# Performance work log

Measured on AMD Instinct MI355X. Metric: run time of the kernel, lower is better.

## Reference

```python
import jax, jax.numpy as jnp
import numpy as np

T, B, I, H, L = 512, 64, 1024, 1024, 2


def setup_inputs() -> dict:
    key = jax.random.key(0)
    ks = jax.random.split(key, 10)
    stdv = 1.0 / np.sqrt(H)
    u = lambda k, shape: jax.random.uniform(k, shape, jnp.float32, -stdv, stdv)
    return {
        "x": jax.random.normal(ks[0], (T, B, I), jnp.float32),
        "hx": jnp.zeros((L, B, H), jnp.float32),
        "cx": jnp.zeros((L, B, H), jnp.float32),
        "w_ih0": u(ks[1], (4 * H, I)),
        "w_hh0": u(ks[2], (4 * H, H)),
        "b_ih0": u(ks[3], (4 * H,)),
        "b_hh0": u(ks[4], (4 * H,)),
        "w_ih1": u(ks[5], (4 * H, H)),
        "w_hh1": u(ks[6], (4 * H, H)),
        "b_ih1": u(ks[7], (4 * H,)),
        "b_hh1": u(ks[8], (4 * H,)),
    }


def _lstm_layer(x, h0, c0, w_ih, w_hh, b_ih, b_hh):
    # Precompute input contribution for all timesteps: [T, B, 4H]
    igates = jnp.einsum("tbi,gi->tbg", x, w_ih) + b_ih

    def step(carry, ig_t):
        h, c = carry
        gates = ig_t + h @ w_hh.T + b_hh
        i, f, g, o = jnp.split(gates, 4, axis=-1)
        i = jax.nn.sigmoid(i)
        f = jax.nn.sigmoid(f)
        g = jnp.tanh(g)
        o = jax.nn.sigmoid(o)
        c = f * c + i * g
        h = o * jnp.tanh(c)
        return (h, c), h

    (hT, cT), out = jax.lax.scan(step, (h0, c0), igates)
    return out, hT, cT


def reference(x, hx, cx, w_ih0, w_hh0, b_ih0, b_hh0, w_ih1, w_hh1, b_ih1, b_hh1):
    params = [(w_ih0, w_hh0, b_ih0, b_hh0), (w_ih1, w_hh1, b_ih1, b_hh1)]
    out = x
    h_final, c_final = [], []
    for layer in range(L):
        out, hT, cT = _lstm_layer(out, hx[layer], cx[layer], *params[layer])
        h_final.append(hT)
        c_final.append(cT)
    hn = jnp.stack(h_final)  # [L, B, H]
    cn = jnp.stack(c_final)  # [L, B, H]
    return out, (hn, cn)
```

## Files before the change

kernel.cpp:

```cpp
#include <hip/hip_runtime.h>
#include <hip/hip_bf16.h>
#include <hip/hip_cooperative_groups.h>
#include <cstddef>

namespace cg = cooperative_groups;

typedef short bf16x8 __attribute__((ext_vector_type(8)));
typedef float f32x4 __attribute__((ext_vector_type(4)));

#define T_STEPS 512
#define BATCH   64
#define DIM     1024
#define BD      (BATCH*DIM)
#define XB_ELEMS ((size_t)T_STEPS*BATCH*DIM)
#define IGSLOT  262144
#define FSTRIDE 16

__device__ __forceinline__ float sigmoidf_(float x) { return 1.f / (1.f + __expf(-x)); }
__device__ __forceinline__ float tanhf_(float x)    { return 2.f / (1.f + __expf(-2.f * x)) - 1.f; }
__device__ __forceinline__ unsigned short f2bf(float f) {
    union { float f; unsigned int u; } v; v.f = f;
    unsigned int u = v.u + 0x7fffu + ((v.u >> 16) & 1u);
    return (unsigned short)(u >> 16);
}

__device__ __forceinline__ unsigned long long coh_load8(const void* p) {
    return __hip_atomic_load((const unsigned long long*)p,
                             __ATOMIC_RELAXED, __HIP_MEMORY_SCOPE_AGENT);
}
__device__ __forceinline__ void coh_store8(void* p, unsigned long long v) {
    __hip_atomic_store((unsigned long long*)p, v,
                       __ATOMIC_RELAXED, __HIP_MEMORY_SCOPE_AGENT);
}

__global__ void __launch_bounds__(512, 2)
lstm_fused(const float* __restrict__ x,
           const float* __restrict__ hx,
           const float* __restrict__ cx,
           const float* __restrict__ w_ih0, const float* __restrict__ w_hh0,
           const float* __restrict__ b_ih0, const float* __restrict__ b_hh0,
           const float* __restrict__ w_ih1, const float* __restrict__ w_hh1,
           const float* __restrict__ b_ih1, const float* __restrict__ b_hh1,
           float* __restrict__ out,
           unsigned short* __restrict__ ws)
{
    unsigned short* xb = ws;
    unsigned short* h0 = ws + XB_ELEMS;
    unsigned short* h1 = h0 + 4 * BD;
    float* ig0 = (float*)(h1 + 2 * BD);
    float* ig1 = ig0 + 2 * IGSLOT;
    unsigned* flags = (unsigned*)(ig1 + 2 * IGSLOT);

    const int tid  = threadIdx.x;
    const int lane = tid & 63;
    const int wave = tid >> 6;
    const int kw   = wave >> 2;
    const int mw   = wave & 3;
    const int bid  = blockIdx.x;
    const int role = bid >> 6;
    const int ug   = bid & 63;
    const int ub   = ug * 16;

    __shared__ __align__(16) unsigned short wB[65536];
    __shared__ __align__(16) unsigned short hstage[64][16];
    __shared__ __align__(16) f32x4 red[4][4][64];

    {
        const float* wm = (role == 0) ? w_ih0 : (role == 1) ? w_hh0
                        : (role == 2) ? w_ih1 : w_hh1;
        for (int idx = tid; idx < 8192; idx += 512) {
            int l  = idx & 63;
            int kc = (idx >> 6) & 31;
            int n  = idx >> 11;
            int c  = l & 15, kq = l >> 4;
            const float* src = wm + (size_t)(n * DIM + ub + c) * DIM + kc * 32 + kq * 8;
            float4 v0 = *(const float4*)(src);
            float4 v1 = *(const float4*)(src + 4);
            unsigned short o[8];
            o[0]=f2bf(v0.x); o[1]=f2bf(v0.y); o[2]=f2bf(v0.z); o[3]=f2bf(v0.w);
            o[4]=f2bf(v1.x); o[5]=f2bf(v1.y); o[6]=f2bf(v1.z); o[7]=f2bf(v1.w);
            *(bf16x8*)(&wB[(size_t)idx * 8]) = *(const bf16x8*)o;
        }
    }

    {
        const int nthr = 512 * gridDim.x;
        const int gtid = bid * 512 + tid;
        const float4* xv = (const float4*)x;
        const int n4 = (int)(XB_ELEMS / 4);
        for (int i = gtid; i < n4; i += nthr) {
            float4 v = xv[i];
            ushort4 o;
            o.x=f2bf(v.x); o.y=f2bf(v.y); o.z=f2bf(v.z); o.w=f2bf(v.w);
            *(ushort4*)(xb + (size_t)i * 4) = o;
        }
    }

    if (role == 1 || role == 3) {
        unsigned short* hdst = (role == 1) ? (h0 + 3 * BD) : (h1 + 1 * BD);
        const float* hsrc = hx + (size_t)(role >> 1) * BD;
        const int kcp0 = ub >> 5, sub0 = ub & 31;
        for (int e = tid; e < 1024; e += 512) {
            int row = e >> 4, uu = e & 15;
            hdst[kcp0 * 2048 + row * 32 + sub0 + uu] = f2bf(hsrc[row * DIM + ub + uu]);
        }
    }

    if (tid == 0)
        __hip_atomic_store(flags + (size_t)((role << 6) | ug) * FSTRIDE, 0u,
                           __ATOMIC_RELAXED, __HIP_MEMORY_SCOPE_AGENT);

    const int col  = lane & 15;
    const int quad = lane >> 4;

    float biasv[4] = {0.f, 0.f, 0.f, 0.f};
    if ((role == 0 || role == 2) && kw == 0) {
        const float* bi = (role == 0) ? b_ih0 : b_ih1;
        const float* bh = (role == 0) ? b_hh0 : b_hh1;
        #pragma unroll
        for (int n = 0; n < 4; ++n) {
            int row = n * DIM + ub + col;
            biasv[n] = bi[row] + bh[row];
        }
    }

    float creg[4] = {0.f, 0.f, 0.f, 0.f};
    if ((role == 1 || role == 3) && kw == 0) {
        const float* csrc = cx + (size_t)(role >> 1) * BD;
        #pragma unroll
        for (int r = 0; r < 4; ++r) {
            int m = mw * 16 + quad * 4 + r;
            creg[r] = csrc[m * DIM + ub + col];
        }
    }

    cg::grid_group grid = cg::this_grid();
    __syncthreads();
    grid.sync();

    const int arow = mw * 16 + col;
    const int kc0  = kw * 16;

    auto poll_ge = [&](const unsigned* f, int target) {
        while ((int)__hip_atomic_load(f, __ATOMIC_RELAXED, __HIP_MEMORY_SCOPE_AGENT) < target)
            __builtin_amdgcn_s_sleep(1);
    };
    auto Fp = [&](int set, int idx) -> unsigned* {
        return flags + (size_t)((set << 6) | idx) * FSTRIDE;
    };
    auto publish = [&](int set, int idx, int val) {
        __hip_atomic_store(Fp(set, idx), (unsigned)val,
                           __ATOMIC_RELAXED, __HIP_MEMORY_SCOPE_AGENT);
    };

    auto gemm_plain = [&](const unsigned short* Ap,
                          f32x4& A0, f32x4& A1, f32x4& A2, f32x4& A3) {
        const unsigned short* Abase = Ap + (size_t)arow * DIM + quad * 8 + kc0 * 32;
        #pragma unroll 8
        for (int k2 = 0; k2 < 16; ++k2) {
            int kc = kc0 + k2;
            bf16x8 a  = *(const bf16x8*)(Abase + k2 * 32);
            bf16x8 b0 = *(const bf16x8*)(&wB[((size_t)(0*32 + kc)*64 + lane)*8]);
            bf16x8 b1 = *(const bf16x8*)(&wB[((size_t)(1*32 + kc)*64 + lane)*8]);
            bf16x8 b2 = *(const bf16x8*)(&wB[((size_t)(2*32 + kc)*64 + lane)*8]);
            bf16x8 b3 = *(const bf16x8*)(&wB[((size_t)(3*32 + kc)*64 + lane)*8]);
            A0 = __builtin_amdgcn_mfma_f32_16x16x32_bf16(a, b0, A0, 0, 0, 0);
            A1 = __builtin_amdgcn_mfma_f32_16x16x32_bf16(a, b1, A1, 0, 0, 0);
            A2 = __builtin_amdgcn_mfma_f32_16x16x32_bf16(a, b2, A2, 0, 0, 0);
            A3 = __builtin_amdgcn_mfma_f32_16x16x32_bf16(a, b3, A3, 0, 0, 0);
        }
    };

    auto gemm_coh = [&](const unsigned short* Ap, const float* igb,
                        f32x4& A0, f32x4& A1, f32x4& A2, f32x4& A3) {
        const unsigned short* Abase = Ap + (size_t)arow * 32 + quad * 8
                                    + (size_t)kc0 * 2048;
        if (igb) {
            union { f32x4 v; unsigned long long q[2]; } g0, g1, g2, g3;
            g0.q[0] = coh_load8(igb + 0*128); g0.q[1] = coh_load8(igb + 1*128);
            g1.q[0] = coh_load8(igb + 2*128); g1.q[1] = coh_load8(igb + 3*128);
            g2.q[0] = coh_load8(igb + 4*128); g2.q[1] = coh_load8(igb + 5*128);
            g3.q[0] = coh_load8(igb + 6*128); g3.q[1] = coh_load8(igb + 7*128);
            A0 = g0.v; A1 = g1.v; A2 = g2.v; A3 = g3.v;
        }
        union U { bf16x8 v; unsigned long long q[2]; };
        U pre[8];
        #pragma unroll
        for (int i = 0; i < 8; ++i) {
            pre[i].q[0] = coh_load8(Abase + (size_t)i * 2048);
            pre[i].q[1] = coh_load8(Abase + (size_t)i * 2048 + 4);
        }
        #pragma unroll
        for (int k2 = 0; k2 < 16; ++k2) {
            U cur = pre[k2 & 7];
            if (k2 < 8) {
                pre[k2 & 7].q[0] = coh_load8(Abase + (size_t)(k2 + 8) * 2048);
                pre[k2 & 7].q[1] = coh_load8(Abase + (size_t)(k2 + 8) * 2048 + 4);
            }
            int kc = kc0 + k2;
            bf16x8 b0 = *(const bf16x8*)(&wB[((size_t)(0*32 + kc)*64 + lane)*8]);
            bf16x8 b1 = *(const bf16x8*)(&wB[((size_t)(1*32 + kc)*64 + lane)*8]);
            bf16x8 b2 = *(const bf16x8*)(&wB[((size_t)(2*32 + kc)*64 + lane)*8]);
            bf16x8 b3 = *(const bf16x8*)(&wB[((size_t)(3*32 + kc)*64 + lane)*8]);
            A0 = __builtin_amdgcn_mfma_f32_16x16x32_bf16(cur.v, b0, A0, 0, 0, 0);
            A1 = __builtin_amdgcn_mfma_f32_16x16x32_bf16(cur.v, b1, A1, 0, 0, 0);
            A2 = __builtin_amdgcn_mfma_f32_16x16x32_bf16(cur.v, b2, A2, 0, 0, 0);
            A3 = __builtin_amdgcn_mfma_f32_16x16x32_bf16(cur.v, b3, A3, 0, 0, 0);
        }
    };

    auto k_reduce = [&](f32x4& A0, f32x4& A1, f32x4& A2, f32x4& A3) {
        if (kw) {
            red[0][mw][lane] = A0; red[1][mw][lane] = A1;
            red[2][mw][lane] = A2; red[3][mw][lane] = A3;
        }
        __syncthreads();
        if (!kw) {
            A0 += red[0][mw][lane]; A1 += red[1][mw][lane];
            A2 += red[2][mw][lane]; A3 += red[3][mw][lane];
        }
    };

    auto dump_ig = [&](float* slot, int set, int t,
                       f32x4 A0, f32x4 A1, f32x4 A2, f32x4 A3) {
        if (!kw) {
            float* base = slot + (size_t)ug * 4096 + (size_t)mw * 1024 + lane * 2;
            union { f32x4 v; unsigned long long q[2]; } u0, u1, u2, u3;
            u0.v = A0; u1.v = A1; u2.v = A2; u3.v = A3;
            coh_store8(base + 0*128, u0.q[0]); coh_store8(base + 1*128, u0.q[1]);
            coh_store8(base + 2*128, u1.q[0]); coh_store8(base + 3*128, u1.q[1]);
            coh_store8(base + 4*128, u2.q[0]); coh_store8(base + 5*128, u2.q[1]);
            coh_store8(base + 6*128, u3.q[0]); coh_store8(base + 7*128, u3.q[1]);
        }
        asm volatile("s_waitcnt vmcnt(0)" ::: "memory");
        __syncthreads();
        if (tid == 0) publish(set, ug, t + 1);
    };

    const int kcp = ub >> 5, sub = ub & 31;

    for (int t = 0; t < T_STEPS; ++t) {
        f32x4 A0 = {0,0,0,0}, A1 = {0,0,0,0}, A2 = {0,0,0,0}, A3 = {0,0,0,0};

        if (role == 0) {
            if (tid == 0) poll_ge(Fp(1, ug), t - 1);
            __syncthreads();
            if (!kw) {
                A0 = f32x4{biasv[0], biasv[0], biasv[0], biasv[0]};
                A1 = f32x4{biasv[1], biasv[1], biasv[1], biasv[1]};
                A2 = f32x4{biasv[2], biasv[2], biasv[2], biasv[2]};
                A3 = f32x4{biasv[3], biasv[3], biasv[3], biasv[3]};
            }
            gemm_plain(xb + (size_t)t * BD, A0, A1, A2, A3);
            k_reduce(A0, A1, A2, A3);
            dump_ig(ig0 + (size_t)(t & 1) * IGSLOT, 0, t, A0, A1, A2, A3);

        } else if (role == 2) {
            if (tid < 64) poll_ge(Fp(1, tid), t + 1);
            else if (tid == 64) poll_ge(Fp(3, ug), t - 1);
            __syncthreads();
            if (!kw) {
                A0 = f32x4{biasv[0], biasv[0], biasv[0], biasv[0]};
                A1 = f32x4{biasv[1], biasv[1], biasv[1], biasv[1]};
                A2 = f32x4{biasv[2], biasv[2], biasv[2], biasv[2]};
                A3 = f32x4{biasv[3], biasv[3], biasv[3], biasv[3]};
            }
            gemm_coh(h0 + (size_t)(t & 3) * BD, nullptr, A0, A1, A2, A3);
            k_reduce(A0, A1, A2, A3);
            dump_ig(ig1 + (size_t)(t & 1) * IGSLOT, 2, t, A0, A1, A2, A3);

        } else {
            if (role == 1) {
                if (tid < 64) poll_ge(Fp(1, tid), t);
                else if (tid < 128) poll_ge(Fp(2, tid - 64), t - 3);
                else if (tid == 128) poll_ge(Fp(0, ug), t + 1);
            } else {
                if (tid < 64) poll_ge(Fp(3, tid), t);
                else if (tid == 64) poll_ge(Fp(2, ug), t + 1);
            }
            __syncthreads();

            unsigned short* hring = (role == 1) ? h0 : h1;
            const unsigned short* hsrc = (role == 1)
                ? (h0 + (size_t)((t - 1) & 3) * BD)
                : (h1 + (size_t)((t - 1) & 1) * BD);
            const float* igb = (!kw)
                ? ((role == 1) ? ig0 : ig1) + (size_t)(t & 1) * IGSLOT
                  + (size_t)ug * 4096 + (size_t)mw * 1024 + lane * 2
                : nullptr;
            gemm_coh(hsrc, igb, A0, A1, A2, A3);
            k_reduce(A0, A1, A2, A3);

            float hreg[4] = {0.f, 0.f, 0.f, 0.f};
            if (!kw) {
                #pragma unroll
                for (int r = 0; r < 4; ++r) {
                    float ig_ = sigmoidf_(A0[r]);
                    float fg_ = sigmoidf_(A1[r]);
                    float gg_ = tanhf_(A2[r]);
                    float og_ = sigmoidf_(A3[r]);
                    float c   = fg_ * creg[r] + ig_ * gg_;
                    creg[r]   = c;
                    float h   = og_ * tanhf_(c);
                    hreg[r]   = h;
                    int m = mw * 16 + quad * 4 + r;
                    hstage[m][col] = f2bf(h);
                }
            }
            __syncthreads();
            unsigned short* hout = hring
                + (size_t)((role == 1) ? (t & 3) : (t & 1)) * BD;
            if (wave == 0) {
                const unsigned long long* src = (const unsigned long long*)&hstage[lane][0];
                unsigned long long v0 = src[0], v1 = src[1], v2 = src[2], v3 = src[3];
                unsigned short* dst = hout + (size_t)kcp * 2048 + (size_t)lane * 32 + sub;
                coh_store8(dst + 0,  v0);
                coh_store8(dst + 4,  v1);
                coh_store8(dst + 8,  v2);
                coh_store8(dst + 12, v3);
                asm volatile("s_waitcnt vmcnt(0)" ::: "memory");
                if (tid == 0) publish(role, ug, t + 1);
            }

            if (!kw) {
                if (role == 3) {
                    #pragma unroll
                    for (int r = 0; r < 4; ++r) {
                        int m = mw * 16 + quad * 4 + r;
                        out[(size_t)t * BD + (size_t)m * DIM + ub + col] = hreg[r];
                        if (t == T_STEPS - 1) {
                            out[(size_t)T_STEPS * BD + 1 * BD + m * DIM + ub + col] = hreg[r];
                            out[(size_t)T_STEPS * BD + 3 * BD + m * DIM + ub + col] = creg[r];
                        }
                    }
                } else if (t == T_STEPS - 1) {
                    #pragma unroll
                    for (int r = 0; r < 4; ++r) {
                        int m = mw * 16 + quad * 4 + r;
                        out[(size_t)T_STEPS * BD + 0 * BD + m * DIM + ub + col] = hreg[r];
                        out[(size_t)T_STEPS * BD + 2 * BD + m * DIM + ub + col] = creg[r];
                    }
                }
            }
        }
    }
}

extern "C" void kernel_launch(void* const* d_in, const int* in_sizes, int n_in,
                              void* d_out, int out_size, void* d_ws, size_t ws_size,
                              hipStream_t stream) {
    const float* x     = (const float*)d_in[0];
    const float* hx    = (const float*)d_in[1];
    const float* cx    = (const float*)d_in[2];
    const float* w_ih0 = (const float*)d_in[3];
    const float* w_hh0 = (const float*)d_in[4];
    const float* b_ih0 = (const float*)d_in[5];
    const float* b_hh0 = (const float*)d_in[6];
    const float* w_ih1 = (const float*)d_in[7];
    const float* w_hh1 = (const float*)d_in[8];
    const float* b_ih1 = (const float*)d_in[9];
    const float* b_hh1 = (const float*)d_in[10];
    float* outp = (float*)d_out;
    unsigned short* wsp = (unsigned short*)d_ws;

    void* args[] = { &x, &hx, &cx, &w_ih0, &w_hh0, &b_ih0, &b_hh0,
                     &w_ih1, &w_hh1, &b_ih1, &b_hh1, &outp, &wsp };
    hipLaunchCooperativeKernel((void*)lstm_fused, dim3(256), dim3(512),
                               args, 0, stream);
}
```

Baseline: 3.548 ms.

## Replace block barriers with per-wave counter flags and shuffle-based h publishing

Cross-block synchronisation changes from one thread storing a step index to every wave atomically incrementing a counter, so consumers wait for a count of 4 per step. Polling now happens inside the waves that need the data, and most block-wide __syncthreads around polling and publishing are removed. The k-split reduction uses a workgroup-scope LDS counter instead of a second barrier. The h output is packed with wave shuffles instead of an LDS staging buffer. This aims to cut barrier latency on the serial recurrence path, but it adds more global atomics and relies on subtle memory ordering through relaxed atomics.

Result: slower. 4.593 ms (+29.5%).

```diff
diff --git a/kernel.cpp b/kernel.cpp
--- a/kernel.cpp
+++ b/kernel.cpp
@@ -62,8 +62,10 @@
     const int ub   = ug * 16;
 
     __shared__ __align__(16) unsigned short wB[65536];
-    __shared__ __align__(16) unsigned short hstage[64][16];
     __shared__ __align__(16) f32x4 red[4][4][64];
+    __shared__ unsigned cnt_rd;
+
+    if (tid == 0) cnt_rd = 0;
 
     {
         const float* wm = (role == 0) ? w_ih0 : (role == 1) ? w_hh0
@@ -141,16 +143,14 @@
     const int arow = mw * 16 + col;
     const int kc0  = kw * 16;
 
-    auto poll_ge = [&](const unsigned* f, int target) {
+    auto poll_cnt = [&](int set, int idx, int target) {
+        const unsigned* f = flags + (size_t)((set << 6) | idx) * FSTRIDE;
         while ((int)__hip_atomic_load(f, __ATOMIC_RELAXED, __HIP_MEMORY_SCOPE_AGENT) < target)
             __builtin_amdgcn_s_sleep(1);
     };
-    auto Fp = [&](int set, int idx) -> unsigned* {
-        return flags + (size_t)((set << 6) | idx) * FSTRIDE;
-    };
-    auto publish = [&](int set, int idx, int val) {
-        __hip_atomic_store(Fp(set, idx), (unsigned)val,
-                           __ATOMIC_RELAXED, __HIP_MEMORY_SCOPE_AGENT);
+    auto cnt_add = [&](int set, int idx) {
+        __hip_atomic_fetch_add(flags + (size_t)((set << 6) | idx) * FSTRIDE, 1u,
+                               __ATOMIC_RELAXED, __HIP_MEMORY_SCOPE_AGENT);
     };
 
     auto gemm_plain = [&](const unsigned short* Ap,
@@ -209,8 +209,11 @@
         }
     };
 
-    auto k_reduce = [&](f32x4& A0, f32x4& A1, f32x4& A2, f32x4& A3) {
+    auto k_reduce = [&](int t, f32x4& A0, f32x4& A1, f32x4& A2, f32x4& A3) {
         if (kw) {
+            while ((int)__hip_atomic_load(&cnt_rd, __ATOMIC_RELAXED,
+                                          __HIP_MEMORY_SCOPE_WORKGROUP) < 4 * t)
+                __builtin_amdgcn_s_sleep(1);
             red[0][mw][lane] = A0; red[1][mw][lane] = A1;
             red[2][mw][lane] = A2; red[3][mw][lane] = A3;
         }
@@ -218,23 +221,24 @@
         if (!kw) {
             A0 += red[0][mw][lane]; A1 += red[1][mw][lane];
             A2 += red[2][mw][lane]; A3 += red[3][mw][lane];
-        }
-    };
-
-    auto dump_ig = [&](float* slot, int set, int t,
+            asm volatile("s_waitcnt lgkmcnt(0)" ::: "memory");
+            if (lane == 0)
+                __hip_atomic_fetch_add(&cnt_rd, 1u, __ATOMIC_RELAXED,
+                                       __HIP_MEMORY_SCOPE_WORKGROUP);
+        }
+    };
+
+    auto dump_ig = [&](float* slot, int set,
                        f32x4 A0, f32x4 A1, f32x4 A2, f32x4 A3) {
-        if (!kw) {
-            float* base = slot + (size_t)ug * 4096 + (size_t)mw * 1024 + lane * 2;
-            union { f32x4 v; unsigned long long q[2]; } u0, u1, u2, u3;
-            u0.v = A0; u1.v = A1; u2.v = A2; u3.v = A3;
-            coh_store8(base + 0*128, u0.q[0]); coh_store8(base + 1*128, u0.q[1]);
-            coh_store8(base + 2*128, u1.q[0]); coh_store8(base + 3*128, u1.q[1]);
-            coh_store8(base + 4*128, u2.q[0]); coh_store8(base + 5*128, u2.q[1]);
-            coh_store8(base + 6*128, u3.q[0]); coh_store8(base + 7*128, u3.q[1]);
-        }
+        float* base = slot + (size_t)ug * 4096 + (size_t)mw * 1024 + lane * 2;
+        union { f32x4 v; unsigned long long q[2]; } u0, u1, u2, u3;
+        u0.v = A0; u1.v = A1; u2.v = A2; u3.v = A3;
+        coh_store8(base + 0*128, u0.q[0]); coh_store8(base + 1*128, u0.q[1]);
+        coh_store8(base + 2*128, u1.q[0]); coh_store8(base + 3*128, u1.q[1]);
+        coh_store8(base + 4*128, u2.q[0]); coh_store8(base + 5*128, u2.q[1]);
+        coh_store8(base + 6*128, u3.q[0]); coh_store8(base + 7*128, u3.q[1]);
         asm volatile("s_waitcnt vmcnt(0)" ::: "memory");
-        __syncthreads();
-        if (tid == 0) publish(set, ug, t + 1);
+        if (lane == 0) cnt_add(set, ug);
     };
 
     const int kcp = ub >> 5, sub = ub & 31;
@@ -243,8 +247,7 @@
         f32x4 A0 = {0,0,0,0}, A1 = {0,0,0,0}, A2 = {0,0,0,0}, A3 = {0,0,0,0};
 
         if (role == 0) {
-            if (tid == 0) poll_ge(Fp(1, ug), t - 1);
-            __syncthreads();
+            if (!kw && lane == 0) poll_cnt(1, ug, 4 * (t - 1));
             if (!kw) {
                 A0 = f32x4{biasv[0], biasv[0], biasv[0], biasv[0]};
                 A1 = f32x4{biasv[1], biasv[1], biasv[1], biasv[1]};
@@ -252,33 +255,42 @@
                 A3 = f32x4{biasv[3], biasv[3], biasv[3], biasv[3]};
             }
             gemm_plain(xb + (size_t)t * BD, A0, A1, A2, A3);
-            k_reduce(A0, A1, A2, A3);
-            dump_ig(ig0 + (size_t)(t & 1) * IGSLOT, 0, t, A0, A1, A2, A3);
+            k_reduce(t, A0, A1, A2, A3);
+            if (!kw) dump_ig(ig0 + (size_t)(t & 1) * IGSLOT, 0, A0, A1, A2, A3);
 
         } else if (role == 2) {
-            if (tid < 64) poll_ge(Fp(1, tid), t + 1);
-            else if (tid == 64) poll_ge(Fp(3, ug), t - 1);
-            __syncthreads();
             if (!kw) {
+                if (lane < 32) poll_cnt(1, lane, 4 * (t + 1));
+                else if (lane == 32) poll_cnt(3, ug, 4 * (t - 1));
                 A0 = f32x4{biasv[0], biasv[0], biasv[0], biasv[0]};
                 A1 = f32x4{biasv[1], biasv[1], biasv[1], biasv[1]};
                 A2 = f32x4{biasv[2], biasv[2], biasv[2], biasv[2]};
                 A3 = f32x4{biasv[3], biasv[3], biasv[3], biasv[3]};
+            } else {
+                if (lane < 32) poll_cnt(1, 32 + lane, 4 * (t + 1));
             }
             gemm_coh(h0 + (size_t)(t & 3) * BD, nullptr, A0, A1, A2, A3);
-            k_reduce(A0, A1, A2, A3);
-            dump_ig(ig1 + (size_t)(t & 1) * IGSLOT, 2, t, A0, A1, A2, A3);
+            k_reduce(t, A0, A1, A2, A3);
+            if (!kw) dump_ig(ig1 + (size_t)(t & 1) * IGSLOT, 2, A0, A1, A2, A3);
 
         } else {
             if (role == 1) {
-                if (tid < 64) poll_ge(Fp(1, tid), t);
-                else if (tid < 128) poll_ge(Fp(2, tid - 64), t - 3);
-                else if (tid == 128) poll_ge(Fp(0, ug), t + 1);
+                if (!kw) {
+                    if (lane < 32) poll_cnt(1, lane, 4 * t);
+                    else { poll_cnt(2, 2*(lane-32),     4*(t-3));
+                           poll_cnt(2, 2*(lane-32) + 1, 4*(t-3)); }
+                    if (lane == 0) poll_cnt(0, ug, 4 * (t + 1));
+                } else {
+                    if (lane < 32) poll_cnt(1, 32 + lane, 4 * t);
+                }
             } else {
-                if (tid < 64) poll_ge(Fp(3, tid), t);
-                else if (tid == 64) poll_ge(Fp(2, ug), t + 1);
-            }
-            __syncthreads();
+                if (!kw) {
+                    if (lane < 32) poll_cnt(3, lane, 4 * t);
+                    else if (lane == 32) poll_cnt(2, ug, 4 * (t + 1));
+                } else {
+                    if (lane < 32) poll_cnt(3, 32 + lane, 4 * t);
+                }
+            }
 
             unsigned short* hring = (role == 1) ? h0 : h1;
             const unsigned short* hsrc = (role == 1)
@@ -289,10 +301,10 @@
                   + (size_t)ug * 4096 + (size_t)mw * 1024 + lane * 2
                 : nullptr;
             gemm_coh(hsrc, igb, A0, A1, A2, A3);
-            k_reduce(A0, A1, A2, A3);
-
-            float hreg[4] = {0.f, 0.f, 0.f, 0.f};
+            k_reduce(t, A0, A1, A2, A3);
+
             if (!kw) {
+                float hreg[4];
                 #pragma unroll
                 for (int r = 0; r < 4; ++r) {
                     float ig_ = sigmoidf_(A0[r]);
@@ -301,44 +313,48 @@
                     float og_ = sigmoidf_(A3[r]);
                     float c   = fg_ * creg[r] + ig_ * gg_;
                     creg[r]   = c;
-                    float h   = og_ * tanhf_(c);
-                    hreg[r]   = h;
-                    int m = mw * 16 + quad * 4 + r;
-                    hstage[m][col] = f2bf(h);
-                }
-            }
-            __syncthreads();
-            unsigned short* hout = hring
-                + (size_t)((role == 1) ? (t & 3) : (t & 1)) * BD;
-            if (wave == 0) {
-                const unsigned long long* src = (const unsigned long long*)&hstage[lane][0];
-                unsigned long long v0 = src[0], v1 = src[1], v2 = src[2], v3 = src[3];
-                unsigned short* dst = hout + (size_t)kcp * 2048 + (size_t)lane * 32 + sub;
-                coh_store8(dst + 0,  v0);
-                coh_store8(dst + 4,  v1);
-                coh_store8(dst + 8,  v2);
-                coh_store8(dst + 12, v3);
+                    hreg[r]   = og_ * tanhf_(c);
+                }
+
+                unsigned short* hout = hring
+                    + (size_t)((role == 1) ? (t & 3) : (t & 1)) * BD;
+                int rw = lane >> 2, c4 = lane & 3;
+                int q2 = rw >> 2, r2 = rw & 3;
+                union { unsigned short u[4]; unsigned long long q; } pk;
+                #pragma unroll
+                for (int j = 0; j < 4; ++j) {
+                    int s = q2 * 16 + 4 * c4 + j;
+                    float v0s = __shfl(hreg[0], s);
+                    float v1s = __shfl(hreg[1], s);
+                    float v2s = __shfl(hreg[2], s);
+                    float v3s = __shfl(hreg[3], s);
+                    float v = (r2 == 0) ? v0s : (r2 == 1) ? v1s
+                            : (r2 == 2) ? v2s : v3s;
+                    pk.u[j] = f2bf(v);
+                }
+                int m = mw * 16 + rw;
+                unsigned short* dst = hout + (size_t)kcp * 2048
+                                    + (size_t)m * 32 + sub + 4 * c4;
+                coh_store8(dst, pk.q);
                 asm volatile("s_waitcnt vmcnt(0)" ::: "memory");
-                if (tid == 0) publish(role, ug, t + 1);
-            }
-
-            if (!kw) {
+                if (lane == 0) cnt_add(role, ug);
+
                 if (role == 3) {
                     #pragma unroll
                     for (int r = 0; r < 4; ++r) {
-                        int m = mw * 16 + quad * 4 + r;
-                        out[(size_t)t * BD + (size_t)m * DIM + ub + col] = hreg[r];
+                        int mm = mw * 16 + quad * 4 + r;
+                        out[(size_t)t * BD + (size_t)mm * DIM + ub + col] = hreg[r];
                         if (t == T_STEPS - 1) {
-                            out[(size_t)T_STEPS * BD + 1 * BD + m * DIM + ub + col] = hreg[r];
-                            out[(size_t)T_STEPS * BD + 3 * BD + m * DIM + ub + col] = creg[r];
+                            out[(size_t)T_STEPS * BD + 1 * BD + mm * DIM + ub + col] = hreg[r];
+                            out[(size_t)T_STEPS * BD + 3 * BD + mm * DIM + ub + col] = creg[r];
                         }
                     }
                 } else if (t == T_STEPS - 1) {
                     #pragma unroll
                     for (int r = 0; r < 4; ++r) {
-                        int m = mw * 16 + quad * 4 + r;
-                        out[(size_t)T_STEPS * BD + 0 * BD + m * DIM + ub + col] = hreg[r];
-                        out[(size_t)T_STEPS * BD + 2 * BD + m * DIM + ub + col] = creg[r];
+                        int mm = mw * 16 + quad * 4 + r;
+                        out[(size_t)T_STEPS * BD + 0 * BD + mm * DIM + ub + col] = hreg[r];
+                        out[(size_t)T_STEPS * BD + 2 * BD + mm * DIM + ub + col] = creg[r];
                     }
                 }
             }
```

## Drop x pre-conversion pass and keep full layer-0 hidden history

Applied to the files above, without the earlier changes.

Removes the grid-wide prologue that converted all of x to bf16 in workspace; the layer-0 input GEMM now reads fp32 x directly and converts to bf16 in registers. The layer-0 hidden ring buffer of 4 slots is replaced by a full T+1 history, so the layer-1 input projection no longer needs the back-pressure wait on role 2 progress and reads h0 with plain (cacheable) loads instead of coherent atomics. This trades a large upfront conversion pass and some synchronisation for doubled x read bandwidth per step and a larger workspace.

After: 5.882 ms. 65.8% more time.

```diff
diff --git a/kernel.cpp b/kernel.cpp
--- a/kernel.cpp
+++ b/kernel.cpp
@@ -12,7 +12,6 @@
 #define BATCH   64
 #define DIM     1024
 #define BD      (BATCH*DIM)
-#define XB_ELEMS ((size_t)T_STEPS*BATCH*DIM)
 #define IGSLOT  262144
 #define FSTRIDE 16
 
@@ -44,9 +43,8 @@
            float* __restrict__ out,
            unsigned short* __restrict__ ws)
 {
-    unsigned short* xb = ws;
-    unsigned short* h0 = ws + XB_ELEMS;
-    unsigned short* h1 = h0 + 4 * BD;
+    unsigned short* h0h = ws;
+    unsigned short* h1  = h0h + (size_t)(T_STEPS + 1) * BD;
     float* ig0 = (float*)(h1 + 2 * BD);
     float* ig1 = ig0 + 2 * IGSLOT;
     unsigned* flags = (unsigned*)(ig1 + 2 * IGSLOT);
@@ -83,21 +81,8 @@
         }
     }
 
-    {
-        const int nthr = 512 * gridDim.x;
-        const int gtid = bid * 512 + tid;
-        const float4* xv = (const float4*)x;
-        const int n4 = (int)(XB_ELEMS / 4);
-        for (int i = gtid; i < n4; i += nthr) {
-            float4 v = xv[i];
-            ushort4 o;
-            o.x=f2bf(v.x); o.y=f2bf(v.y); o.z=f2bf(v.z); o.w=f2bf(v.w);
-            *(ushort4*)(xb + (size_t)i * 4) = o;
-        }
-    }
-
     if (role == 1 || role == 3) {
-        unsigned short* hdst = (role == 1) ? (h0 + 3 * BD) : (h1 + 1 * BD);
+        unsigned short* hdst = (role == 1) ? h0h : (h1 + 1 * BD);
         const float* hsrc = hx + (size_t)(role >> 1) * BD;
         const int kcp0 = ub >> 5, sub0 = ub & 31;
         for (int e = tid; e < 1024; e += 512) {
@@ -152,14 +137,22 @@
         __hip_atomic_store(Fp(set, idx), (unsigned)val,
                            __ATOMIC_RELAXED, __HIP_MEMORY_SCOPE_AGENT);
     };
-
-    auto gemm_plain = [&](const unsigned short* Ap,
-                          f32x4& A0, f32x4& A1, f32x4& A2, f32x4& A3) {
-        const unsigned short* Abase = Ap + (size_t)arow * DIM + quad * 8 + kc0 * 32;
-        #pragma unroll 8
+    auto h0_at = [&](int t) -> unsigned short* {
+        return h0h + (size_t)(t + 1) * BD;
+    };
+
+    auto gemm_x = [&](const float* Ap,
+                      f32x4& A0, f32x4& A1, f32x4& A2, f32x4& A3) {
+        const float* Abase = Ap + (size_t)arow * DIM + quad * 8 + kc0 * 32;
+        #pragma unroll 4
         for (int k2 = 0; k2 < 16; ++k2) {
             int kc = kc0 + k2;
-            bf16x8 a  = *(const bf16x8*)(Abase + k2 * 32);
+            float4 v0 = *(const float4*)(Abase + k2 * 32);
+            float4 v1 = *(const float4*)(Abase + k2 * 32 + 4);
+            unsigned short o[8];
+            o[0]=f2bf(v0.x); o[1]=f2bf(v0.y); o[2]=f2bf(v0.z); o[3]=f2bf(v0.w);
+            o[4]=f2bf(v1.x); o[5]=f2bf(v1.y); o[6]=f2bf(v1.z); o[7]=f2bf(v1.w);
+            bf16x8 a = *(const bf16x8*)o;
             bf16x8 b0 = *(const bf16x8*)(&wB[((size_t)(0*32 + kc)*64 + lane)*8]);
             bf16x8 b1 = *(const bf16x8*)(&wB[((size_t)(1*32 + kc)*64 + lane)*8]);
             bf16x8 b2 = *(const bf16x8*)(&wB[((size_t)(2*32 + kc)*64 + lane)*8]);
@@ -168,6 +161,39 @@
             A1 = __builtin_amdgcn_mfma_f32_16x16x32_bf16(a, b1, A1, 0, 0, 0);
             A2 = __builtin_amdgcn_mfma_f32_16x16x32_bf16(a, b2, A2, 0, 0, 0);
             A3 = __builtin_amdgcn_mfma_f32_16x16x32_bf16(a, b3, A3, 0, 0, 0);
+        }
+    };
+
+    auto gemm_cached = [&](const unsigned short* Ap, const float* igb,
+                           f32x4& A0, f32x4& A1, f32x4& A2, f32x4& A3) {
+        const unsigned short* Abase = Ap + (size_t)arow * 32 + quad * 8
+                                    + (size_t)kc0 * 2048;
+        if (igb) {
+            union { f32x4 v; unsigned long long q[2]; } g0, g1, g2, g3;
+            g0.q[0] = coh_load8(igb + 0*128); g0.q[1] = coh_load8(igb + 1*128);
+            g1.q[0] = coh_load8(igb + 2*128); g1.q[1] = coh_load8(igb + 3*128);
+            g2.q[0] = coh_load8(igb + 4*128); g2.q[1] = coh_load8(igb + 5*128);
+            g3.q[0] = coh_load8(igb + 6*128); g3.q[1] = coh_load8(igb + 7*128);
+            A0 = g0.v; A1 = g1.v; A2 = g2.v; A3 = g3.v;
+        }
+        bf16x8 pre[8];
+        #pragma unroll
+        for (int i = 0; i < 8; ++i)
+            pre[i] = *(const bf16x8*)(Abase + (size_t)i * 2048);
+        #pragma unroll
+        for (int k2 = 0; k2 < 16; ++k2) {
+            bf16x8 cur = pre[k2 & 7];
+            if (k2 < 8)
+                pre[k2 & 7] = *(const bf16x8*)(Abase + (size_t)(k2 + 8) * 2048);
+            int kc = kc0 + k2;
+            bf16x8 b0 = *(const bf16x8*)(&wB[((size_t)(0*32 + kc)*64 + lane)*8]);
+            bf16x8 b1 = *(const bf16x8*)(&wB[((size_t)(1*32 + kc)*64 + lane)*8]);
+            bf16x8 b2 = *(const bf16x8*)(&wB[((size_t)(2*32 + kc)*64 + lane)*8]);
+            bf16x8 b3 = *(const bf16x8*)(&wB[((size_t)(3*32 + kc)*64 + lane)*8]);
+            A0 = __builtin_amdgcn_mfma_f32_16x16x32_bf16(cur, b0, A0, 0, 0, 0);
+            A1 = __builtin_amdgcn_mfma_f32_16x16x32_bf16(cur, b1, A1, 0, 0, 0);
+            A2 = __builtin_amdgcn_mfma_f32_16x16x32_bf16(cur, b2, A2, 0, 0, 0);
+            A3 = __builtin_amdgcn_mfma_f32_16x16x32_bf16(cur, b3, A3, 0, 0, 0);
         }
     };
 
@@ -251,7 +277,7 @@
                 A2 = f32x4{biasv[2], biasv[2], biasv[2], biasv[2]};
                 A3 = f32x4{biasv[3], biasv[3], biasv[3], biasv[3]};
             }
-            gemm_plain(xb + (size_t)t * BD, A0, A1, A2, A3);
+            gemm_x(x + (size_t)t * BD, A0, A1, A2, A3);
             k_reduce(A0, A1, A2, A3);
             dump_ig(ig0 + (size_t)(t & 1) * IGSLOT, 0, t, A0, A1, A2, A3);
 
@@ -265,30 +291,20 @@
                 A2 = f32x4{biasv[2], biasv[2], biasv[2], biasv[2]};
                 A3 = f32x4{biasv[3], biasv[3], biasv[3], biasv[3]};
             }
-            gemm_coh(h0 + (size_t)(t & 3) * BD, nullptr, A0, A1, A2, A3);
+            gemm_cached(h0_at(t), nullptr, A0, A1, A2, A3);
             k_reduce(A0, A1, A2, A3);
             dump_ig(ig1 + (size_t)(t & 1) * IGSLOT, 2, t, A0, A1, A2, A3);
 
-        } else {
-            if (role == 1) {
-                if (tid < 64) poll_ge(Fp(1, tid), t);
-                else if (tid < 128) poll_ge(Fp(2, tid - 64), t - 3);
-                else if (tid == 128) poll_ge(Fp(0, ug), t + 1);
-            } else {
-                if (tid < 64) poll_ge(Fp(3, tid), t);
-                else if (tid == 64) poll_ge(Fp(2, ug), t + 1);
-            }
-            __syncthreads();
-
-            unsigned short* hring = (role == 1) ? h0 : h1;
-            const unsigned short* hsrc = (role == 1)
-                ? (h0 + (size_t)((t - 1) & 3) * BD)
-                : (h1 + (size_t)((t - 1) & 1) * BD);
+        } else if (role == 1) {
+            if (tid < 64) poll_ge(Fp(1, tid), t);
+            else if (tid == 64) poll_ge(Fp(0, ug), t + 1);
+            __syncthreads();
+
             const float* igb = (!kw)
-                ? ((role == 1) ? ig0 : ig1) + (size_t)(t & 1) * IGSLOT
+                ? ig0 + (size_t)(t & 1) * IGSLOT
                   + (size_t)ug * 4096 + (size_t)mw * 1024 + lane * 2
                 : nullptr;
-            gemm_coh(hsrc, igb, A0, A1, A2, A3);
+            gemm_cached(h0_at(t - 1), igb, A0, A1, A2, A3);
             k_reduce(A0, A1, A2, A3);
 
             float hreg[4] = {0.f, 0.f, 0.f, 0.f};
@@ -308,8 +324,57 @@
                 }
             }
             __syncthreads();
-            unsigned short* hout = hring
-                + (size_t)((role == 1) ? (t & 3) : (t & 1)) * BD;
+            if (wave == 0) {
+                const unsigned long long* src = (const unsigned long long*)&hstage[lane][0];
+                unsigned long long v0 = src[0], v1 = src[1], v2 = src[2], v3 = src[3];
+                unsigned short* dst = h0_at(t) + (size_t)kcp * 2048
+                                    + (size_t)lane * 32 + sub;
+                coh_store8(dst + 0,  v0);
+                coh_store8(dst + 4,  v1);
+                coh_store8(dst + 8,  v2);
+                coh_store8(dst + 12, v3);
+                asm volatile("s_waitcnt vmcnt(0)" ::: "memory");
+                if (tid == 0) publish(1, ug, t + 1);
+            }
+            if (!kw && t == T_STEPS - 1) {
+                #pragma unroll
+                for (int r = 0; r < 4; ++r) {
+                    int m = mw * 16 + quad * 4 + r;
+                    out[(size_t)T_STEPS * BD + 0 * BD + m * DIM + ub + col] = hreg[r];
+                    out[(size_t)T_STEPS * BD + 2 * BD + m * DIM + ub + col] = creg[r];
+                }
+            }
+
+        } else {
+            if (tid < 64) poll_ge(Fp(3, tid), t);
+            else if (tid == 64) poll_ge(Fp(2, ug), t + 1);
+            __syncthreads();
+
+            const float* igb = (!kw)
+                ? ig1 + (size_t)(t & 1) * IGSLOT
+                  + (size_t)ug * 4096 + (size_t)mw * 1024 + lane * 2
+                : nullptr;
+            gemm_coh(h1 + (size_t)((t - 1) & 1) * BD, igb, A0, A1, A2, A3);
+            k_reduce(A0, A1, A2, A3);
+
+            float hreg[4] = {0.f, 0.f, 0.f, 0.f};
+            if (!kw) {
+                #pragma unroll
+                for (int r = 0; r < 4; ++r) {
+                    float ig_ = sigmoidf_(A0[r]);
+                    float fg_ = sigmoidf_(A1[r]);
+                    float gg_ = tanhf_(A2[r]);
+                    float og_ = sigmoidf_(A3[r]);
+                    float c   = fg_ * creg[r] + ig_ * gg_;
+                    creg[r]   = c;
+                    float h   = og_ * tanhf_(c);
+                    hreg[r]   = h;
+                    int m = mw * 16 + quad * 4 + r;
+                    hstage[m][col] = f2bf(h);
+                }
+            }
+            __syncthreads();
+            unsigned short* hout = h1 + (size_t)(t & 1) * BD;
             if (wave == 0) {
                 const unsigned long long* src = (const unsigned long long*)&hstage[lane][0];
                 unsigned long long v0 = src[0], v1 = src[1], v2 = src[2], v3 = src[3];
@@ -319,26 +384,17 @@
                 coh_store8(dst + 8,  v2);
                 coh_store8(dst + 12, v3);
                 asm volatile("s_waitcnt vmcnt(0)" ::: "memory");
-                if (tid == 0) publish(role, ug, t + 1);
+                if (tid == 0) publish(3, ug, t + 1);
             }
 
             if (!kw) {
-                if (role == 3) {
-                    #pragma unroll
-                    for (int r = 0; r < 4; ++r) {
-                        int m = mw * 16 + quad * 4 + r;
-                        out[(size_t)t * BD + (size_t)m * DIM + ub + col] = hreg[r];
-                        if (t == T_STEPS - 1) {
-                            out[(size_t)T_STEPS * BD + 1 * BD + m * DIM + ub + col] = hreg[r];
-                            out[(size_t)T_STEPS * BD + 3 * BD + m * DIM + ub + col] = creg[r];
-                        }
-                    }
-                } else if (t == T_STEPS - 1) {
-                    #pragma unroll
-                    for (int r = 0; r < 4; ++r) {
-                        int m = mw * 16 + quad * 4 + r;
-                        out[(size_t)T_STEPS * BD + 0 * BD + m * DIM + ub + col] = hreg[r];
-                        out[(size_t)T_STEPS * BD + 2 * BD + m * DIM + ub + col] = creg[r];
+                #pragma unroll
+                for (int r = 0; r < 4; ++r) {
+                    int m = mw * 16 + quad * 4 + r;
+                    out[(size_t)t * BD + (size_t)m * DIM + ub + col] = hreg[r];
+                    if (t == T_STEPS - 1) {
+                        out[(size_t)T_STEPS * BD + 1 * BD + m * DIM + ub + col] = hreg[r];
+                        out[(size_t)T_STEPS * BD + 3 * BD + m * DIM + ub + col] = creg[r];
                     }
                 }
             }
```
